# Kernel optimization log

Hardware: AMD Instinct MI355X
Metric: run time of the kernel (lower is better)

## Reference

```python
import jax, jax.numpy as jnp
import numpy as np


def _hippo_dplr(n):
    # HiPPO-LegS -> NPLR -> DPLR (diagonal plus low rank) init, as in S4
    pr = np.sqrt(1.0 + 2.0 * np.arange(n))
    A = -(np.tril(pr[:, None] * pr[None, :]) - np.diag(np.arange(n)))
    p = np.sqrt(np.arange(n) + 0.5)
    b = np.sqrt(2.0 * np.arange(n) + 1.0)
    S = A + p[:, None] * p[None, :]
    lam_re = np.full(n, np.mean(np.diagonal(S)))
    lam_im, V = np.linalg.eigh(S * -1j)  # S*-1j is Hermitian
    p_c = V.conj().T @ p.astype(np.complex128)
    b_c = V.conj().T @ b.astype(np.complex128)
    return lam_re, lam_im, p_c, b_c


def setup_inputs():
    B, L, H, N = 4, 1024, 512, 64
    key = jax.random.key(0)
    kx, kc, ks, k1, k2 = jax.random.split(key, 5)
    lam_re, lam_im, p_c, b_c = _hippo_dplr(N)
    c = jax.random.normal(kc, (N, 2)) * (0.5 ** 0.5)
    f32 = lambda a: jnp.asarray(a, dtype=jnp.float32)
    return {
        'x': jax.random.normal(kx, (B, L, H), dtype=jnp.float32),
        'norm_weight': jnp.ones((H,), jnp.float32),
        'norm_bias': jnp.zeros((H,), jnp.float32),
        'lambda_re': f32(lam_re), 'lambda_im': f32(lam_im),
        'p_re': f32(p_c.real), 'p_im': f32(p_c.imag),
        'b_re': f32(b_c.real), 'b_im': f32(b_c.imag),
        'c_re': c[:, 0].astype(jnp.float32), 'c_im': c[:, 1].astype(jnp.float32),
        'd': jnp.ones((), jnp.float32),
        'log_step': jax.random.uniform(ks, (), jnp.float32, float(np.log(0.001)), float(np.log(0.1))),
        'out_w': (jax.random.normal(k1, (H, H), jnp.float32) / np.sqrt(H)).astype(jnp.float32),
        'out_b': jnp.zeros((H,), jnp.float32),
        'out2_w': (jax.random.normal(k2, (H, H), jnp.float32) / np.sqrt(H)).astype(jnp.float32),
        'out2_b': jnp.zeros((H,), jnp.float32),
    }


def reference(x, norm_weight, norm_bias, lambda_re, lambda_im, p_re, p_im,
              b_re, b_im, c_re, c_im, d, log_step, out_w, out_b, out2_w, out2_b):
    Bsz, L, H = x.shape
    skip = x
    # LayerNorm over channel dim (eps=1e-5, eqx default)
    mu = jnp.mean(x, -1, keepdims=True)
    var = jnp.mean((x - mu) ** 2, -1, keepdims=True)
    xn = (x - mu) / jnp.sqrt(var + 1e-5) * norm_weight + norm_bias
    # --- S4 DPLR bilinear discretization ---
    lam = (lambda_re + 1j * lambda_im).astype(jnp.complex64)
    p = (p_re + 1j * p_im).astype(jnp.complex64)
    b = (b_re + 1j * b_im).astype(jnp.complex64)
    c = (c_re + 1j * c_im).astype(jnp.complex64)
    step = jnp.exp(log_step).astype(jnp.complex64)
    N = lam.shape[0]
    I = jnp.eye(N, dtype=jnp.complex64)
    A = jnp.diag(lam) - p[:, None] * p[None, :].conj()
    A0 = (2.0 / step) * I + A
    Dinv = jnp.diag(1.0 / ((2.0 / step) - lam))
    qcD = p.conj()[None, :] @ Dinv           # [1,N]
    Dp = Dinv @ p[:, None]                   # [N,1]
    A1 = Dinv - (Dp @ qcD) / (1.0 + (qcD @ p[:, None]))  # Woodbury
    Ab = A1 @ A0                             # [N,N] discrete state matrix
    Bb = 2.0 * (A1 @ b[:, None])[:, 0]       # [N]
    # --- sequential state-space scan over time, vectorized over (B,H) lanes ---
    u = xn.astype(jnp.complex64)             # [B,L,H]

    def step_fn(state, u_t):                 # state: [B,H,N], u_t: [B,H]
        new = jnp.einsum('nm,bhm->bhn', Ab, state) + u_t[..., None] * Bb
        return new, jnp.einsum('n,bhn->bh', c, new).real

    init = jnp.zeros((Bsz, H, N), jnp.complex64)
    _, ys = jax.lax.scan(step_fn, init, jnp.moveaxis(u, 1, 0))  # ys: [L,B,H]
    y = jnp.moveaxis(ys, 0, 1) + d * xn      # feedthrough term
    # --- GELU + GLU-style gated output projection, residual ---
    y = jax.nn.gelu(y)
    gate = jax.nn.sigmoid(y @ out2_w.T + out2_b)
    return skip + (y @ out_w.T + out_b) * gate
```

## Files before the change

### kernel.cpp

```cpp
#include <hip/hip_runtime.h>
#include <hip/hip_bf16.h>
#include <math.h>

#define HDIM 512
#define LSEQ 1024
#define BSZ  4

typedef __attribute__((ext_vector_type(8))) short short8;
typedef __attribute__((ext_vector_type(4))) float floatx4;

__device__ __forceinline__ float2 cmul(float2 a, float2 b) {
  float2 r;
  r.x = a.x * b.x - a.y * b.y;
  r.y = a.x * b.y + a.y * b.x;
  return r;
}
__device__ __forceinline__ float2 cadd(float2 a, float2 b) {
  float2 r; r.x = a.x + b.x; r.y = a.y + b.y; return r;
}
__device__ __forceinline__ float2 cfma(float2 a, float2 b, float2 c) {
  c.x += a.x * b.x - a.y * b.y;
  c.y += a.x * b.y + a.y * b.x;
  return c;
}
__device__ __forceinline__ ushort f2bf(float f) {
  __hip_bfloat16 h = __float2bfloat16(f);
  return *(ushort*)&h;
}

__global__ __launch_bounds__(576) void stage1_kernel(
    const float* __restrict__ x, const float* __restrict__ nw,
    const float* __restrict__ nb, float* __restrict__ xn,
    const float* __restrict__ lre, const float* __restrict__ lim,
    const float* __restrict__ pre, const float* __restrict__ pim,
    const float* __restrict__ bre, const float* __restrict__ bim,
    const float* __restrict__ cre, const float* __restrict__ cim,
    const float* __restrict__ logstep, float* __restrict__ Kout,
    const float* __restrict__ w1, const float* __restrict__ w2,
    ushort* __restrict__ Wst) {
  __shared__ float2 Ldab[64], Lu[64], Lr[64], LBb[64];
  __shared__ float2 Rv[2048];
  __shared__ float2 Wv[2048];
  int tid = threadIdx.x;
  int wv = tid >> 6;
  int lane = tid & 63;

  if (blockIdx.x != 0) {
    int row = (blockIdx.x - 1) * 9 + wv;
    if (row < BSZ * LSEQ) {
      const float* xr = x + (size_t)row * HDIM;
      float4 v0 = ((const float4*)xr)[lane];
      float4 v1 = ((const float4*)xr)[lane + 64];
      float s  = v0.x + v0.y + v0.z + v0.w + v1.x + v1.y + v1.z + v1.w;
      float ss = v0.x*v0.x + v0.y*v0.y + v0.z*v0.z + v0.w*v0.w
               + v1.x*v1.x + v1.y*v1.y + v1.z*v1.z + v1.w*v1.w;
      #pragma unroll
      for (int m = 1; m < 64; m <<= 1) { s += __shfl_xor(s, m); ss += __shfl_xor(ss, m); }
      float mu   = s * (1.0f / HDIM);
      float var  = ss * (1.0f / HDIM) - mu * mu;
      float rstd = rsqrtf(var + 1e-5f);
      float4 w0 = ((const float4*)nw)[lane];
      float4 w1v = ((const float4*)nw)[lane + 64];
      float4 b0 = ((const float4*)nb)[lane];
      float4 b1 = ((const float4*)nb)[lane + 64];
      float4 o0, o1;
      o0.x = (v0.x - mu) * rstd * w0.x + b0.x;
      o0.y = (v0.y - mu) * rstd * w0.y + b0.y;
      o0.z = (v0.z - mu) * rstd * w0.z + b0.z;
      o0.w = (v0.w - mu) * rstd * w0.w + b0.w;
      o1.x = (v1.x - mu) * rstd * w1v.x + b1.x;
      o1.y = (v1.y - mu) * rstd * w1v.y + b1.y;
      o1.z = (v1.z - mu) * rstd * w1v.z + b1.z;
      o1.w = (v1.w - mu) * rstd * w1v.w + b1.w;
      float* xo = xn + (size_t)row * HDIM;
      ((float4*)xo)[lane] = o0;
      ((float4*)xo)[lane + 64] = o1;
    }
    int idx = (blockIdx.x - 1) * 576 + tid;
    if (idx < 65536) {
      int e0 = idx * 8;
      int n = e0 >> 9, k0 = e0 & 511;
      const float* Wr = (n < 512) ? (w1 + (size_t)n * 512 + k0)
                                  : (w2 + (size_t)(n - 512) * 512 + k0);
      ushort tmp[8];
      #pragma unroll
      for (int q = 0; q < 8; q++) tmp[q] = f2bf(Wr[q]);
      *(short8*)&Wst[e0] = *(short8*)tmp;
    }
    return;
  }

  if (tid < 64) {
    int n = tid;
    float step = expf(logstep[0]);
    float g = 2.0f / step;
    float lr = lre[n], li = lim[n];
    float pr = pre[n], pi = pim[n];
    float br = bre[n], bi = bim[n];
    float den  = (g - lr) * (g - lr) + li * li;
    float dinr = (g - lr) / den, dini = li / den;
    float dabr = (g + lr) * dinr - li * dini;
    float dabi = (g + lr) * dini + li * dinr;
    float ur = dinr * pr - dini * pi;
    float ui = dinr * pi + dini * pr;
    float qr = pr * dinr + pi * dini;
    float qi = pr * dini - pi * dinr;
    float pm2 = pr * pr + pi * pi;
    float betr = pm2 * dinr, beti = pm2 * dini;
    float gar = qr * br - qi * bi;
    float gai = qr * bi + qi * br;
    #pragma unroll
    for (int m = 1; m < 64; m <<= 1) {
      betr += __shfl_xor(betr, m); beti += __shfl_xor(beti, m);
      gar  += __shfl_xor(gar, m);  gai  += __shfl_xor(gai, m);
    }
    float obr = 1.0f + betr, obi = beti;
    float ob2 = obr * obr + obi * obi;
    float kr = -2.0f * g * obr / ob2;
    float ki =  2.0f * g * obi / ob2;
    float rr = kr * qr - ki * qi;
    float ri = kr * qi + ki * qr;
    float tgr = (gar * obr + gai * obi) / ob2;
    float tgi = (gai * obr - gar * obi) / ob2;
    float dbr = dinr * br - dini * bi;
    float dbi = dinr * bi + dini * br;
    float Bbr = 2.0f * (dbr - (ur * tgr - ui * tgi));
    float Bbi = 2.0f * (dbi - (ur * tgi + ui * tgr));
    float2 t;
    t.x = dabr; t.y = dabi; Ldab[n] = t;
    t.x = ur;   t.y = ui;   Lu[n]   = t;
    t.x = rr;   t.y = ri;   Lr[n]   = t;
    t.x = Bbr;  t.y = Bbi;  LBb[n]  = t;
  }
  if (wv == 8) { float2 cc; cc.x = cre[lane]; cc.y = cim[lane]; Rv[lane] = cc; }
  __syncthreads();

  int g8 = lane >> 3;
  int q8 = lane & 7;
  int jm = wv * 8 + g8;
  float2 cv[8];

  if (wv < 8) {
    float2 dab[8], u[8], rn[8];
    #pragma unroll
    for (int ii = 0; ii < 8; ii++) {
      int n = q8 * 8 + ii;
      dab[ii] = Ldab[n]; u[ii] = Lu[n]; rn[ii] = Lr[n];
    }
    float2 rj = Lr[jm];
    #pragma unroll
    for (int ii = 0; ii < 8; ii++) {
      int n = q8 * 8 + ii;
      cv[ii] = cmul(u[ii], rj);
      if (n == jm) cv[ii] = cadd(cv[ii], dab[ii]);
    }
    for (int s = 0; s < 31; s++) {
      float2 part; part.x = 0.f; part.y = 0.f;
      #pragma unroll
      for (int ii = 0; ii < 8; ii++) part = cfma(rn[ii], cv[ii], part);
      #pragma unroll
      for (int m = 1; m < 8; m <<= 1) {
        part.x += __shfl_xor(part.x, m);
        part.y += __shfl_xor(part.y, m);
      }
      #pragma unroll
      for (int ii = 0; ii < 8; ii++) {
        float2 nc = cmul(dab[ii], cv[ii]);
        cv[ii] = cfma(u[ii], part, nc);
      }
    }
  } else {
    float2 dab0 = Ldab[lane], u0 = Lu[lane], r0 = Lr[lane];
    float2 w = LBb[lane];
    Wv[lane * 32 + 0] = w;
    for (int b = 1; b < 32; b++) {
      float dr = r0.x * w.x - r0.y * w.y;
      float di = r0.x * w.y + r0.y * w.x;
      #pragma unroll
      for (int m = 1; m < 64; m <<= 1) { dr += __shfl_xor(dr, m); di += __shfl_xor(di, m); }
      float2 nw2;
      nw2.x = dab0.x * w.x - dab0.y * w.y + u0.x * dr - u0.y * di;
      nw2.y = dab0.x * w.y + dab0.y * w.x + u0.x * di + u0.y * dr;
      w = nw2;
      Wv[lane * 32 + b] = w;
    }
  }
  __syncthreads();

  for (int a = 1; a < 32; a++) {
    if (wv < 8) {
      float2 part; part.x = 0.f; part.y = 0.f;
      #pragma unroll
      for (int ii = 0; ii < 8; ii++) {
        float2 Rk = Rv[(a - 1) * 64 + q8 * 8 + ii];
        part = cfma(Rk, cv[ii], part);
      }
      #pragma unroll
      for (int m = 1; m < 8; m <<= 1) {
        part.x += __shfl_xor(part.x, m);
        part.y += __shfl_xor(part.y, m);
      }
      if (q8 == 0) Rv[a * 64 + jm] = part;
    }
    __syncthreads();
  }

  for (int midx = tid; midx < 1024; midx += 576) {
    int a = midx >> 5, b = midx & 31;
    float acc = 0.f;
    for (int n = 0; n < 64; n++) {
      float2 R = Rv[a * 64 + n];
      float2 W = Wv[n * 32 + b];
      acc += R.x * W.x - R.y * W.y;
    }
    Kout[midx] = acc;
  }
}

__global__ __launch_bounds__(256) void prep_kernel(
    const float* __restrict__ xn, const float* __restrict__ K,
    ushort* __restrict__ Uhi,
    ushort* __restrict__ Thi, ushort* __restrict__ Tlo) {
  __shared__ float tile[64][65];
  int blk = blockIdx.x;
  int tid = threadIdx.x;
  if (blk < 512) {
    int ht = blk & 7, lt = (blk >> 3) & 15, b = blk >> 7;
    #pragma unroll
    for (int q = 0; q < 16; q++) {
      int idx = q * 256 + tid;
      int r = idx >> 6, c = idx & 63;
      tile[r][c] = xn[((size_t)(b * LSEQ + lt * 64 + r)) * HDIM + ht * 64 + c];
    }
    __syncthreads();
    #pragma unroll
    for (int q = 0; q < 16; q++) {
      int idx = q * 256 + tid;
      int r = idx >> 6, c = idx & 63;
      size_t off = ((size_t)(b * HDIM + ht * 64 + r)) * LSEQ + lt * 64 + c;
      Uhi[off] = f2bf(tile[c][r]);
    }
  } else {
    int r = blk - 512;
    int t = r * 2 + (tid >> 7);
    int tau0 = (tid & 127) * 8;
    ushort hi[8], lo[8];
    #pragma unroll
    for (int q = 0; q < 8; q++) {
      int tau = tau0 + q;
      float v = (tau <= t) ? K[t - tau] : 0.f;
      hi[q] = f2bf(v);
      float rem = v - __bfloat162float(*(__hip_bfloat16*)&hi[q]);
      lo[q] = f2bf(rem);
    }
    *(short8*)&Thi[(size_t)t * 1024 + tau0] = *(short8*)hi;
    *(short8*)&Tlo[(size_t)t * 1024 + tau0] = *(short8*)lo;
  }
}

__global__ __launch_bounds__(256) void conv_gemm_kernel(
    const ushort* __restrict__ Thi, const ushort* __restrict__ Tlo,
    const ushort* __restrict__ Uhi,
    const float* __restrict__ xn, const float* __restrict__ dptr,
    __hip_bfloat16* __restrict__ A) {
  __shared__ ushort sbuf[2 * 7680];
  int tid = threadIdx.x;
  int lane = tid & 63;
  int wv = tid >> 6;
  int wm = wv >> 1, wn = wv & 1;
  int by = blockIdx.y;
  int bm = (by < 8) ? by : 23 - by;
  int bn = blockIdx.x;
  floatx4 acc[2][2] = {};
  int srow = tid >> 2;
  int scol = (tid & 3) * 8;
  int ldst = srow * 40 + scol;
  int fr = lane & 15, fq = (lane >> 4) * 8;
  size_t Toff = (size_t)(bm * 64 + srow) * 1024 + scol;
  size_t Uoff = (size_t)(bn * 64 + srow) * 1024 + scol;
  int KT = 2 * (bm + 1);
  {
    uint4 th = *(const uint4*)&Thi[Toff];
    uint4 tl = *(const uint4*)&Tlo[Toff];
    uint4 uh = *(const uint4*)&Uhi[Uoff];
    *(uint4*)&sbuf[ldst]        = th;
    *(uint4*)&sbuf[ldst + 2560] = tl;
    *(uint4*)&sbuf[ldst + 5120] = uh;
  }
  __syncthreads();
  for (int kt = 0; kt < KT; kt++) {
    int cur = kt & 1;
    uint4 nth = {}, ntl = {}, nuh = {};
    if (kt + 1 < KT) {
      size_t k1 = (size_t)(kt + 1) * 32;
      nth = *(const uint4*)&Thi[Toff + k1];
      ntl = *(const uint4*)&Tlo[Toff + k1];
      nuh = *(const uint4*)&Uhi[Uoff + k1];
    }
    const ushort* sTh = sbuf + cur * 7680;
    const ushort* sTl = sTh + 2560;
    const ushort* sUh = sTh + 5120;
    short8 ah[2], al[2], bh[2];
    #pragma unroll
    for (int i = 0; i < 2; i++) {
      ah[i] = *(const short8*)&sTh[(wm * 32 + i * 16 + fr) * 40 + fq];
      al[i] = *(const short8*)&sTl[(wm * 32 + i * 16 + fr) * 40 + fq];
      bh[i] = *(const short8*)&sUh[(wn * 32 + i * 16 + fr) * 40 + fq];
    }
    #pragma unroll
    for (int i = 0; i < 2; i++)
      #pragma unroll
      for (int j = 0; j < 2; j++) {
        acc[i][j] = __builtin_amdgcn_mfma_f32_16x16x32_bf16(ah[i], bh[j], acc[i][j], 0, 0, 0);
        acc[i][j] = __builtin_amdgcn_mfma_f32_16x16x32_bf16(al[i], bh[j], acc[i][j], 0, 0, 0);
      }
    if (kt + 1 < KT) {
      ushort* dst = sbuf + (cur ^ 1) * 7680;
      *(uint4*)&dst[ldst]        = nth;
      *(uint4*)&dst[ldst + 2560] = ntl;
      *(uint4*)&dst[ldst + 5120] = nuh;
      __syncthreads();
    }
  }
  float d = dptr[0];
  int row0 = bm * 64 + wm * 32;
  int col0 = bn * 64 + wn * 32;
  int fc = lane & 15, frq = (lane >> 4) * 4;
  #pragma unroll
  for (int i = 0; i < 2; i++)
    #pragma unroll
    for (int j = 0; j < 2; j++)
      #pragma unroll
      for (int r = 0; r < 4; r++) {
        int t = row0 + i * 16 + frq + r;
        int c = col0 + j * 16 + fc;
        int b = c >> 9, h = c & 511;
        size_t off = (size_t)(b * LSEQ + t) * HDIM + h;
        float y = acc[i][j][r] + d * xn[off];
        float tnh = tanhf(0.7978845608028654f * (y + 0.044715f * y * y * y));
        A[off] = __float2bfloat16(0.5f * y * (1.0f + tnh));
      }
}

__global__ __launch_bounds__(256) void proj_kernel(
    const __hip_bfloat16* __restrict__ Abuf, const ushort* __restrict__ Wst,
    const float* __restrict__ x, const float* __restrict__ ob,
    const float* __restrict__ o2b, float* __restrict__ out) {
  __shared__ ushort sbuf[2 * 7680];
  int tid = threadIdx.x;
  int lane = tid & 63;
  int wv = tid >> 6;
  int wm = wv >> 1, wn = wv & 1;
  int bm = blockIdx.y, bn = blockIdx.x;
  int srow = tid >> 2;
  int scol = (tid & 3) * 8;
  int ldst = srow * 40 + scol;
  int fr = lane & 15, fq = (lane >> 4) * 8;
  floatx4 acc1[2][2] = {}, acc2[2][2] = {};
  const ushort* Ab = (const ushort*)Abuf;
  size_t Aoff  = (size_t)(bm * 64 + srow) * 512 + scol;
  size_t W1off = (size_t)(bn * 64 + srow) * 512 + scol;
  size_t W2off = W1off + (size_t)512 * 512;
  {
    uint4 a0 = *(const uint4*)&Ab[Aoff];
    uint4 v1 = *(const uint4*)&Wst[W1off];
    uint4 v2 = *(const uint4*)&Wst[W2off];
    *(uint4*)&sbuf[ldst]        = a0;
    *(uint4*)&sbuf[ldst + 2560] = v1;
    *(uint4*)&sbuf[ldst + 5120] = v2;
  }
  __syncthreads();
  for (int kt = 0; kt < 16; kt++) {
    int cur = kt & 1;
    uint4 na = {}, n1 = {}, n2 = {};
    if (kt + 1 < 16) {
      int k1 = (kt + 1) * 32;
      na = *(const uint4*)&Ab[Aoff + k1];
      n1 = *(const uint4*)&Wst[W1off + k1];
      n2 = *(const uint4*)&Wst[W2off + k1];
    }
    const ushort* sA  = sbuf + cur * 7680;
    const ushort* sW1 = sA + 2560;
    const ushort* sW2 = sA + 5120;
    short8 af[2], b1[2], b2[2];
    #pragma unroll
    for (int i = 0; i < 2; i++) {
      af[i] = *(const short8*)&sA[(wm * 32 + i * 16 + fr) * 40 + fq];
      b1[i] = *(const short8*)&sW1[(wn * 32 + i * 16 + fr) * 40 + fq];
      b2[i] = *(const short8*)&sW2[(wn * 32 + i * 16 + fr) * 40 + fq];
    }
    #pragma unroll
    for (int i = 0; i < 2; i++)
      #pragma unroll
      for (int j = 0; j < 2; j++) {
        acc1[i][j] = __builtin_amdgcn_mfma_f32_16x16x32_bf16(af[i], b1[j], acc1[i][j], 0, 0, 0);
        acc2[i][j] = __builtin_amdgcn_mfma_f32_16x16x32_bf16(af[i], b2[j], acc2[i][j], 0, 0, 0);
      }
    if (kt + 1 < 16) {
      ushort* dst = sbuf + (cur ^ 1) * 7680;
      *(uint4*)&dst[ldst]        = na;
      *(uint4*)&dst[ldst + 2560] = n1;
      *(uint4*)&dst[ldst + 5120] = n2;
      __syncthreads();
    }
  }
  int row0 = bm * 64 + wm * 32;
  int col0 = bn * 64 + wn * 32;
  int fc = lane & 15, frq = (lane >> 4) * 4;
  #pragma unroll
  for (int i = 0; i < 2; i++)
    #pragma unroll
    for (int j = 0; j < 2; j++)
      #pragma unroll
      for (int r = 0; r < 4; r++) {
        int row = row0 + i * 16 + frq + r;
        int col = col0 + j * 16 + fc;
        float c1 = acc1[i][j][r] + ob[col];
        float c2 = acc2[i][j][r] + o2b[col];
        float gate = 1.0f / (1.0f + expf(-c2));
        size_t off = (size_t)row * HDIM + col;
        out[off] = x[off] + c1 * gate;
      }
}

extern "C" void kernel_launch(void* const* d_in, const int* in_sizes, int n_in,
                              void* d_out, int out_size, void* d_ws, size_t ws_size,
                              hipStream_t stream) {
  const float* x   = (const float*)d_in[0];
  const float* nw  = (const float*)d_in[1];
  const float* nb  = (const float*)d_in[2];
  const float* lre = (const float*)d_in[3];
  const float* lim = (const float*)d_in[4];
  const float* pre = (const float*)d_in[5];
  const float* pim = (const float*)d_in[6];
  const float* bre = (const float*)d_in[7];
  const float* bim = (const float*)d_in[8];
  const float* cre = (const float*)d_in[9];
  const float* cim = (const float*)d_in[10];
  const float* dsc = (const float*)d_in[11];
  const float* lst = (const float*)d_in[12];
  const float* w1  = (const float*)d_in[13];
  const float* ob  = (const float*)d_in[14];
  const float* w2  = (const float*)d_in[15];
  const float* o2b = (const float*)d_in[16];

  char* ws = (char*)d_ws;
  float* xn    = (float*)(ws);
  ushort* Uhi  = (ushort*)(ws + (size_t)(8  << 20));
  ushort* Thi  = (ushort*)(ws + (size_t)(12 << 20));
  ushort* Tlo  = (ushort*)(ws + (size_t)(14 << 20));
  ushort* Wst  = (ushort*)(ws + (size_t)(16 << 20));
  __hip_bfloat16* Abuf = (__hip_bfloat16*)(ws + (size_t)(17 << 20));
  float* Kbuf  = (float*)(ws + (size_t)(21 << 20));
  float* out   = (float*)d_out;

  stage1_kernel<<<dim3(457), dim3(576), 0, stream>>>(x, nw, nb, xn,
                                                     lre, lim, pre, pim, bre, bim,
                                                     cre, cim, lst, Kbuf,
                                                     w1, w2, Wst);
  prep_kernel<<<dim3(1024), dim3(256), 0, stream>>>(xn, Kbuf, Uhi, Thi, Tlo);
  conv_gemm_kernel<<<dim3(32, 16), dim3(256), 0, stream>>>(Thi, Tlo, Uhi,
                                                           xn, dsc, Abuf);
  proj_kernel<<<dim3(8, 64), dim3(256), 0, stream>>>(Abuf, Wst, x, ob, o2b, out);
}
```

Before: 165.5 us.

## Fuse prep kernel into stage1 using an inter-block flag for the Toeplitz build

```diff
diff --git a/kernel.cpp b/kernel.cpp
--- a/kernel.cpp
+++ b/kernel.cpp
@@ -5,6 +5,7 @@
 #define HDIM 512
 #define LSEQ 1024
 #define BSZ  4
+#define KFLAG_MAGIC 0x13579BDFu
 
 typedef __attribute__((ext_vector_type(8))) short short8;
 typedef __attribute__((ext_vector_type(4))) float floatx4;
@@ -37,7 +38,9 @@
     const float* __restrict__ cre, const float* __restrict__ cim,
     const float* __restrict__ logstep, float* __restrict__ Kout,
     const float* __restrict__ w1, const float* __restrict__ w2,
-    ushort* __restrict__ Wst) {
+    ushort* __restrict__ Wst, ushort* __restrict__ Uhi,
+    ushort* __restrict__ Thi, ushort* __restrict__ Tlo,
+    unsigned int* __restrict__ kflag) {
   __shared__ float2 Ldab[64], Lu[64], Lr[64], LBb[64];
   __shared__ float2 Rv[2048];
   __shared__ float2 Wv[2048];
@@ -75,6 +78,16 @@
       float* xo = xn + (size_t)row * HDIM;
       ((float4*)xo)[lane] = o0;
       ((float4*)xo)[lane + 64] = o1;
+      int b = row >> 10, t = row & 1023;
+      ushort* ub = Uhi + ((size_t)(b * 512 + lane * 4)) * 1024 + t;
+      ub[0]                  = f2bf(o0.x);
+      ub[1024]               = f2bf(o0.y);
+      ub[2048]               = f2bf(o0.z);
+      ub[3072]               = f2bf(o0.w);
+      ub[(size_t)256 * 1024] = f2bf(o1.x);
+      ub[(size_t)257 * 1024] = f2bf(o1.y);
+      ub[(size_t)258 * 1024] = f2bf(o1.z);
+      ub[(size_t)259 * 1024] = f2bf(o1.w);
     }
     int idx = (blockIdx.x - 1) * 576 + tid;
     if (idx < 65536) {
@@ -86,6 +99,30 @@
       #pragma unroll
       for (int q = 0; q < 8; q++) tmp[q] = f2bf(Wr[q]);
       *(short8*)&Wst[e0] = *(short8*)tmp;
+    }
+    if (blockIdx.x <= 256) {
+      if (tid == 0) {
+        while (__hip_atomic_load(kflag, __ATOMIC_ACQUIRE,
+                                 __HIP_MEMORY_SCOPE_AGENT) != KFLAG_MAGIC) {
+          __builtin_amdgcn_s_sleep(16);
+        }
+      }
+      __syncthreads();
+      if (tid < 512) {
+        int t = (blockIdx.x - 1) * 4 + (tid >> 7);
+        int tau0 = (tid & 127) * 8;
+        ushort hi[8], lo[8];
+        #pragma unroll
+        for (int q = 0; q < 8; q++) {
+          int tau = tau0 + q;
+          float v = (tau <= t) ? Kout[t - tau] : 0.f;
+          hi[q] = f2bf(v);
+          float rem = v - __bfloat162float(*(__hip_bfloat16*)&hi[q]);
+          lo[q] = f2bf(rem);
+        }
+        *(short8*)&Thi[(size_t)t * 1024 + tau0] = *(short8*)hi;
+        *(short8*)&Tlo[(size_t)t * 1024 + tau0] = *(short8*)lo;
+      }
     }
     return;
   }
@@ -215,46 +252,10 @@
     }
     Kout[midx] = acc;
   }
-}
-
-__global__ __launch_bounds__(256) void prep_kernel(
-    const float* __restrict__ xn, const float* __restrict__ K,
-    ushort* __restrict__ Uhi,
-    ushort* __restrict__ Thi, ushort* __restrict__ Tlo) {
-  __shared__ float tile[64][65];
-  int blk = blockIdx.x;
-  int tid = threadIdx.x;
-  if (blk < 512) {
-    int ht = blk & 7, lt = (blk >> 3) & 15, b = blk >> 7;
-    #pragma unroll
-    for (int q = 0; q < 16; q++) {
-      int idx = q * 256 + tid;
-      int r = idx >> 6, c = idx & 63;
-      tile[r][c] = xn[((size_t)(b * LSEQ + lt * 64 + r)) * HDIM + ht * 64 + c];
-    }
-    __syncthreads();
-    #pragma unroll
-    for (int q = 0; q < 16; q++) {
-      int idx = q * 256 + tid;
-      int r = idx >> 6, c = idx & 63;
-      size_t off = ((size_t)(b * HDIM + ht * 64 + r)) * LSEQ + lt * 64 + c;
-      Uhi[off] = f2bf(tile[c][r]);
-    }
-  } else {
-    int r = blk - 512;
-    int t = r * 2 + (tid >> 7);
-    int tau0 = (tid & 127) * 8;
-    ushort hi[8], lo[8];
-    #pragma unroll
-    for (int q = 0; q < 8; q++) {
-      int tau = tau0 + q;
-      float v = (tau <= t) ? K[t - tau] : 0.f;
-      hi[q] = f2bf(v);
-      float rem = v - __bfloat162float(*(__hip_bfloat16*)&hi[q]);
-      lo[q] = f2bf(rem);
-    }
-    *(short8*)&Thi[(size_t)t * 1024 + tau0] = *(short8*)hi;
-    *(short8*)&Tlo[(size_t)t * 1024 + tau0] = *(short8*)lo;
+  __syncthreads();
+  if (tid == 0) {
+    __threadfence();
+    __hip_atomic_store(kflag, KFLAG_MAGIC, __ATOMIC_RELEASE, __HIP_MEMORY_SCOPE_AGENT);
   }
 }
 
@@ -452,13 +453,14 @@
   ushort* Wst  = (ushort*)(ws + (size_t)(16 << 20));
   __hip_bfloat16* Abuf = (__hip_bfloat16*)(ws + (size_t)(17 << 20));
   float* Kbuf  = (float*)(ws + (size_t)(21 << 20));
+  unsigned int* kflag = (unsigned int*)(ws + (size_t)(21 << 20) + 4096);
   float* out   = (float*)d_out;
 
   stage1_kernel<<<dim3(457), dim3(576), 0, stream>>>(x, nw, nb, xn,
                                                      lre, lim, pre, pim, bre, bim,
                                                      cre, cim, lst, Kbuf,
-                                                     w1, w2, Wst);
-  prep_kernel<<<dim3(1024), dim3(256), 0, stream>>>(xn, Kbuf, Uhi, Thi, Tlo);
+                                                     w1, w2, Wst, Uhi, Thi, Tlo,
+                                                     kflag);
   conv_gemm_kernel<<<dim3(32, 16), dim3(256), 0, stream>>>(Thi, Tlo, Uhi,
                                                            xn, dsc, Abuf);
   proj_kernel<<<dim3(8, 64), dim3(256), 0, stream>>>(Abuf, Wst, x, ob, o2b, out);
```

New measurement: 178.2 us. +7.7%, slower.

## Fuse Toeplitz and input bf16 prep into conv GEMM loads

Applied to the files above, without the earlier changes.

```diff
diff --git a/kernel.cpp b/kernel.cpp
--- a/kernel.cpp
+++ b/kernel.cpp
@@ -26,6 +26,9 @@
 __device__ __forceinline__ ushort f2bf(float f) {
   __hip_bfloat16 h = __float2bfloat16(f);
   return *(ushort*)&h;
+}
+__device__ __forceinline__ float bf2f(ushort u) {
+  return __bfloat162float(*(__hip_bfloat16*)&u);
 }
 
 __global__ __launch_bounds__(576) void stage1_kernel(
@@ -217,52 +220,9 @@
   }
 }
 
-__global__ __launch_bounds__(256) void prep_kernel(
-    const float* __restrict__ xn, const float* __restrict__ K,
-    ushort* __restrict__ Uhi,
-    ushort* __restrict__ Thi, ushort* __restrict__ Tlo) {
-  __shared__ float tile[64][65];
-  int blk = blockIdx.x;
-  int tid = threadIdx.x;
-  if (blk < 512) {
-    int ht = blk & 7, lt = (blk >> 3) & 15, b = blk >> 7;
-    #pragma unroll
-    for (int q = 0; q < 16; q++) {
-      int idx = q * 256 + tid;
-      int r = idx >> 6, c = idx & 63;
-      tile[r][c] = xn[((size_t)(b * LSEQ + lt * 64 + r)) * HDIM + ht * 64 + c];
-    }
-    __syncthreads();
-    #pragma unroll
-    for (int q = 0; q < 16; q++) {
-      int idx = q * 256 + tid;
-      int r = idx >> 6, c = idx & 63;
-      size_t off = ((size_t)(b * HDIM + ht * 64 + r)) * LSEQ + lt * 64 + c;
-      Uhi[off] = f2bf(tile[c][r]);
-    }
-  } else {
-    int r = blk - 512;
-    int t = r * 2 + (tid >> 7);
-    int tau0 = (tid & 127) * 8;
-    ushort hi[8], lo[8];
-    #pragma unroll
-    for (int q = 0; q < 8; q++) {
-      int tau = tau0 + q;
-      float v = (tau <= t) ? K[t - tau] : 0.f;
-      hi[q] = f2bf(v);
-      float rem = v - __bfloat162float(*(__hip_bfloat16*)&hi[q]);
-      lo[q] = f2bf(rem);
-    }
-    *(short8*)&Thi[(size_t)t * 1024 + tau0] = *(short8*)hi;
-    *(short8*)&Tlo[(size_t)t * 1024 + tau0] = *(short8*)lo;
-  }
-}
-
 __global__ __launch_bounds__(256) void conv_gemm_kernel(
-    const ushort* __restrict__ Thi, const ushort* __restrict__ Tlo,
-    const ushort* __restrict__ Uhi,
-    const float* __restrict__ xn, const float* __restrict__ dptr,
-    __hip_bfloat16* __restrict__ A) {
+    const float* __restrict__ K, const float* __restrict__ xn,
+    const float* __restrict__ dptr, __hip_bfloat16* __restrict__ A) {
   __shared__ ushort sbuf[2 * 7680];
   int tid = threadIdx.x;
   int lane = tid & 63;
@@ -276,26 +236,42 @@
   int scol = (tid & 3) * 8;
   int ldst = srow * 40 + scol;
   int fr = lane & 15, fq = (lane >> 4) * 8;
-  size_t Toff = (size_t)(bm * 64 + srow) * 1024 + scol;
-  size_t Uoff = (size_t)(bn * 64 + srow) * 1024 + scol;
+  int trow = bm * 64 + srow;
+  int tbase = trow - scol;
+  int c = bn * 64 + srow;
+  const float* xrow = xn + ((size_t)(c >> 9) * LSEQ) * HDIM + (c & 511);
   int KT = 2 * (bm + 1);
+
+  float tv[8], uv[8];
+  #pragma unroll
+  for (int i = 0; i < 8; i++) {
+    int idx = tbase - i;
+    tv[i] = (idx >= 0) ? K[idx] : 0.f;
+    uv[i] = xrow[(size_t)(scol + i) * HDIM];
+  }
   {
-    uint4 th = *(const uint4*)&Thi[Toff];
-    uint4 tl = *(const uint4*)&Tlo[Toff];
-    uint4 uh = *(const uint4*)&Uhi[Uoff];
-    *(uint4*)&sbuf[ldst]        = th;
-    *(uint4*)&sbuf[ldst + 2560] = tl;
-    *(uint4*)&sbuf[ldst + 5120] = uh;
+    ushort th[8], tl[8], uu[8];
+    #pragma unroll
+    for (int i = 0; i < 8; i++) {
+      th[i] = f2bf(tv[i]);
+      tl[i] = f2bf(tv[i] - bf2f(th[i]));
+      uu[i] = f2bf(uv[i]);
+    }
+    *(short8*)&sbuf[ldst]        = *(short8*)th;
+    *(short8*)&sbuf[ldst + 2560] = *(short8*)tl;
+    *(short8*)&sbuf[ldst + 5120] = *(short8*)uu;
   }
   __syncthreads();
   for (int kt = 0; kt < KT; kt++) {
     int cur = kt & 1;
-    uint4 nth = {}, ntl = {}, nuh = {};
     if (kt + 1 < KT) {
-      size_t k1 = (size_t)(kt + 1) * 32;
-      nth = *(const uint4*)&Thi[Toff + k1];
-      ntl = *(const uint4*)&Tlo[Toff + k1];
-      nuh = *(const uint4*)&Uhi[Uoff + k1];
+      int k0 = (kt + 1) * 32;
+      #pragma unroll
+      for (int i = 0; i < 8; i++) {
+        int idx = tbase - k0 - i;
+        tv[i] = (idx >= 0) ? K[idx] : 0.f;
+        uv[i] = xrow[(size_t)(k0 + scol + i) * HDIM];
+      }
     }
     const ushort* sTh = sbuf + cur * 7680;
     const ushort* sTl = sTh + 2560;
@@ -315,10 +291,17 @@
         acc[i][j] = __builtin_amdgcn_mfma_f32_16x16x32_bf16(al[i], bh[j], acc[i][j], 0, 0, 0);
       }
     if (kt + 1 < KT) {
+      ushort th[8], tl[8], uu[8];
+      #pragma unroll
+      for (int i = 0; i < 8; i++) {
+        th[i] = f2bf(tv[i]);
+        tl[i] = f2bf(tv[i] - bf2f(th[i]));
+        uu[i] = f2bf(uv[i]);
+      }
       ushort* dst = sbuf + (cur ^ 1) * 7680;
-      *(uint4*)&dst[ldst]        = nth;
-      *(uint4*)&dst[ldst + 2560] = ntl;
-      *(uint4*)&dst[ldst + 5120] = nuh;
+      *(short8*)&dst[ldst]        = *(short8*)th;
+      *(short8*)&dst[ldst + 2560] = *(short8*)tl;
+      *(short8*)&dst[ldst + 5120] = *(short8*)uu;
       __syncthreads();
     }
   }
@@ -333,8 +316,8 @@
       #pragma unroll
       for (int r = 0; r < 4; r++) {
         int t = row0 + i * 16 + frq + r;
-        int c = col0 + j * 16 + fc;
-        int b = c >> 9, h = c & 511;
+        int cc = col0 + j * 16 + fc;
+        int b = cc >> 9, h = cc & 511;
         size_t off = (size_t)(b * LSEQ + t) * HDIM + h;
         float y = acc[i][j][r] + d * xn[off];
         float tnh = tanhf(0.7978845608028654f * (y + 0.044715f * y * y * y));
@@ -446,20 +429,15 @@
 
   char* ws = (char*)d_ws;
   float* xn    = (float*)(ws);
-  ushort* Uhi  = (ushort*)(ws + (size_t)(8  << 20));
-  ushort* Thi  = (ushort*)(ws + (size_t)(12 << 20));
-  ushort* Tlo  = (ushort*)(ws + (size_t)(14 << 20));
-  ushort* Wst  = (ushort*)(ws + (size_t)(16 << 20));
-  __hip_bfloat16* Abuf = (__hip_bfloat16*)(ws + (size_t)(17 << 20));
-  float* Kbuf  = (float*)(ws + (size_t)(21 << 20));
+  ushort* Wst  = (ushort*)(ws + (size_t)(8 << 20));
+  __hip_bfloat16* Abuf = (__hip_bfloat16*)(ws + (size_t)(9 << 20));
+  float* Kbuf  = (float*)(ws + (size_t)(13 << 20));
   float* out   = (float*)d_out;
 
   stage1_kernel<<<dim3(457), dim3(576), 0, stream>>>(x, nw, nb, xn,
                                                      lre, lim, pre, pim, bre, bim,
                                                      cre, cim, lst, Kbuf,
                                                      w1, w2, Wst);
-  prep_kernel<<<dim3(1024), dim3(256), 0, stream>>>(xn, Kbuf, Uhi, Thi, Tlo);
-  conv_gemm_kernel<<<dim3(32, 16), dim3(256), 0, stream>>>(Thi, Tlo, Uhi,
-                                                           xn, dsc, Abuf);
+  conv_gemm_kernel<<<dim3(32, 16), dim3(256), 0, stream>>>(Kbuf, xn, dsc, Abuf);
   proj_kernel<<<dim3(8, 64), dim3(256), 0, stream>>>(Abuf, Wst, x, ob, o2b, out);
 }
```

Result: slower. 180.0 us (+8.8%).
